# Kernel tuning notes

Measured on AMD Instinct MI355X. Metric: run time of the kernel, lower is better.

Reference implementation:

```python
import jax, jax.numpy as jnp
import numpy as np

B, N, F, C, E = 32768, 14, 128, 128, 64
NEG_SLOPE = 0.2

def setup_inputs() -> dict:
    key = jax.random.key(0)
    ks = jax.random.split(key, 14)
    feature = jax.random.normal(ks[0], (B, N, F), jnp.float32)
    src = jax.random.randint(ks[1], (B, E), 0, N)
    off = jax.random.randint(ks[2], (B, E), 1, N)
    dst = (src + off) % N  # guaranteed no self loops
    edge_list = jnp.stack([src, dst], axis=-1)  # [B,E,2] (src,dst) pairs
    s = 0.1
    return {
        'feature': feature,
        'edge_list': edge_list,
        'W1': jax.random.normal(ks[3], (F, C), jnp.float32) * s,
        'a_s1': jax.random.normal(ks[4], (C,), jnp.float32) * s,
        'a_d1': jax.random.normal(ks[5], (C,), jnp.float32) * s,
        'b1': jnp.zeros((C,), jnp.float32),
        'W2': jax.random.normal(ks[6], (C, C), jnp.float32) * s,
        'a_s2': jax.random.normal(ks[7], (C,), jnp.float32) * s,
        'a_d2': jax.random.normal(ks[8], (C,), jnp.float32) * s,
        'b2': jnp.zeros((C,), jnp.float32),
        'Wl': jax.random.normal(ks[9], (N * C, C // 2), jnp.float32) * 0.02,
        'bl': jnp.zeros((C // 2,), jnp.float32),
        'Wp': jax.random.normal(ks[10], (C // 2, 1), jnp.float32) * 0.02,
        'bp': jnp.zeros((1,), jnp.float32),
    }

def _gat_layer(x, W, a_s, a_d, b, src, dst):
    # x: [B,N,Fin]; src,dst: [B,Et] (self loops included). PyG GATConv, 1 head.
    Bn, Nn, _ = x.shape
    Et = src.shape[1]
    h = x @ W                                   # [B,N,C]
    as_n = jnp.einsum('bnc,c->bn', h, a_s)      # per-node src score
    ad_n = jnp.einsum('bnc,c->bn', h, a_d)      # per-node dst score
    logit = jax.nn.leaky_relu(
        jnp.take_along_axis(as_n, src, axis=1) + jnp.take_along_axis(ad_n, dst, axis=1),
        NEG_SLOPE)                               # [B,Et]
    # edge softmax grouped by (graph, dst) via flat segment ids
    seg = (jnp.arange(Bn)[:, None] * Nn + dst).reshape(-1)   # [B*Et]
    lf = logit.reshape(-1)
    m = jnp.full((Bn * Nn,), -jnp.inf, lf.dtype).at[seg].max(lf)
    e = jnp.exp(lf - m[seg])
    z = jnp.zeros((Bn * Nn,), lf.dtype).at[seg].add(e)
    alpha = e / z[seg]                           # [B*Et]
    Cc = h.shape[-1]
    msg = jnp.take_along_axis(h, src[..., None], axis=1).reshape(Bn * Et, Cc) * alpha[:, None]
    out = jnp.zeros((Bn * Nn, Cc), h.dtype).at[seg].add(msg).reshape(Bn, Nn, Cc) + b
    return out, alpha.reshape(Bn, Et)

def reference(feature, edge_list, W1, a_s1, a_d1, b1, W2, a_s2, a_d2, b2, Wl, bl, Wp, bp):
    Bn = feature.shape[0]
    sl = jnp.broadcast_to(jnp.arange(N)[None, :], (Bn, N))
    src = jnp.concatenate([edge_list[..., 0], sl], axis=1)   # [B,E+N]
    dst = jnp.concatenate([edge_list[..., 1], sl], axis=1)
    h1, _ = _gat_layer(feature, W1, a_s1, a_d1, b1, src, dst)
    h1 = jax.nn.relu(h1)                         # dropout p=0 (eval)
    h2, alpha = _gat_layer(h1, W2, a_s2, a_d2, b2, src, dst)
    attn = jnp.zeros((Bn, N, N), feature.dtype).at[jnp.arange(Bn)[:, None], src, dst].set(alpha)
    x = h2.reshape(Bn, N * C) @ Wl + bl
    pred = jax.nn.sigmoid(x @ Wp + bp)           # [B,1]
    return pred, attn
```

## Files before the change

### kernel.cpp

```cpp
#include <hip/hip_runtime.h>


#define NEG_SLOPE 0.2f

typedef __bf16 bf16x8 __attribute__((ext_vector_type(8)));
typedef float f32x4 __attribute__((ext_vector_type(4)));
typedef unsigned short us4v __attribute__((ext_vector_type(4)));
typedef unsigned short us8v __attribute__((ext_vector_type(8)));

static __device__ __forceinline__ unsigned short f2bf(float f) {
  unsigned u = __builtin_bit_cast(unsigned, f);
  return (unsigned short)((u + 0x7FFFu + ((u >> 16) & 1u)) >> 16);
}

__global__ void gat_setup_kernel(const float* __restrict__ W1, const float* __restrict__ W2,
                                 const float* __restrict__ Wl, const float* __restrict__ bl,
                                 const float* __restrict__ Wp, const float* __restrict__ bp,
                                 unsigned short* __restrict__ wfrag, float* __restrict__ weffc) {
  const int blk = blockIdx.x, tid = threadIdx.x;
  if (blk < 16) {
    int slot = blk * 256 + tid;
    int lane = slot & 63, t = (slot >> 6) & 7, ks = (slot >> 9) & 3, lr = slot >> 11;
    const float* W = lr ? W2 : W1;
    int q = lane >> 4, l = lane & 15;
    int n = t * 16 + l, k0 = ks * 32 + q * 8;
    us8v hv;
    #pragma unroll
    for (int j = 0; j < 8; ++j) hv[j] = f2bf(W[(k0 + j) * 128 + n]);
    *(us8v*)(wfrag + slot * 8) = hv;
  } else {
    for (int i = tid; i < 2048; i += 256) {
      int r = i & 3, lane = (i >> 2) & 63, t = i >> 8;
      int q = lane >> 4, l = lane & 15;
      int row = 4 * q + r, col = t * 16 + l;
      float s = 0.f;
      if (row < 14) {
        const float* wl = Wl + (size_t)(row * 128 + col) * 64;
        #pragma unroll 8
        for (int c = 0; c < 64; ++c) s += wl[c] * Wp[c];
      }
      weffc[i] = s;
    }
    if (tid == 0) {
      float s = 0.f;
      for (int c = 0; c < 64; ++c) s += bl[c] * Wp[c];
      weffc[2048] = s + bp[0];
    }
  }
}

struct __align__(16) WaveLds {
  unsigned short xh[3072];
  unsigned short Pb[384];
  float Pf[256];
  float asn[16], adn[16], mz[16];
  float attn[196];
};

__global__ __launch_bounds__(256, 4) void gat_kernel(
    const float* __restrict__ feat, const int* __restrict__ edges,
    const float* __restrict__ as1v, const float* __restrict__ ad1v,
    const float* __restrict__ b1v, const float* __restrict__ as2v,
    const float* __restrict__ ad2v, const float* __restrict__ b2v,
    const unsigned short* __restrict__ wfrag, const float* __restrict__ weffc,
    float* __restrict__ out) {
  __shared__ WaveLds wls[4];
  const int tid = threadIdx.x;
  const int wave = tid >> 6, lane = tid & 63;
  const int q = lane >> 4, l = lane & 15;
  const int g = blockIdx.x * 4 + wave;
  WaveLds& S = wls[wave];

  int esrc, edst;
  { const int2 e2 = *(const int2*)(edges + (size_t)g * 128 + lane * 2); esrc = e2.x; edst = e2.y; }

  us8v z8v = {0, 0, 0, 0, 0, 0, 0, 0};
  const bf16x8 zf = __builtin_bit_cast(bf16x8, z8v);

  bf16x8 af1[4];
  if (l < 14) {
    const float* fb = feat + (size_t)g * 1792 + l * 128 + q * 8;
    #pragma unroll
    for (int ks = 0; ks < 4; ++ks) {
      f32x4 v0 = *(const f32x4*)(fb + ks * 32);
      f32x4 v1 = *(const f32x4*)(fb + ks * 32 + 4);
      us8v hv;
      hv[0] = f2bf(v0[0]); hv[1] = f2bf(v0[1]); hv[2] = f2bf(v0[2]); hv[3] = f2bf(v0[3]);
      hv[4] = f2bf(v1[0]); hv[5] = f2bf(v1[1]); hv[6] = f2bf(v1[2]); hv[7] = f2bf(v1[3]);
      af1[ks] = __builtin_bit_cast(bf16x8, hv);
    }
  } else {
    #pragma unroll
    for (int ks = 0; ks < 4; ++ks) af1[ks] = zf;
  }

  f32x4 oacc[8];

  for (int lr = 0; lr < 2; ++lr) {
    const float* asv = lr ? as2v : as1v;
    const float* adv = lr ? ad2v : ad1v;
    const float* bsv = lr ? b2v : b1v;
    const unsigned short* wfl = wfrag + lr * 16384;

    f32x4 hacc[8];
    #pragma unroll
    for (int t = 0; t < 8; ++t) hacc[t] = (f32x4){0.f, 0.f, 0.f, 0.f};
    #pragma unroll
    for (int ks = 0; ks < 4; ++ks) {
      bf16x8 af = lr ? *(const bf16x8*)(&S.xh[l * 136 + ks * 32 + q * 8]) : af1[ks];
      const unsigned short* wk = wfl + ks * 4096 + lane * 8;
      #pragma unroll
      for (int t = 0; t < 8; ++t) {
        bf16x8 bfv = *(const bf16x8*)(wk + t * 512);
        hacc[t] = __builtin_amdgcn_mfma_f32_16x16x32_bf16(af, bfv, hacc[t], 0, 0, 0);
      }
    }

    f32x4 pas = {0.f, 0.f, 0.f, 0.f}, padv = {0.f, 0.f, 0.f, 0.f};
    #pragma unroll
    for (int t = 0; t < 8; ++t) {
      float ca = asv[t * 16 + l], cd = adv[t * 16 + l];
      pas += hacc[t] * ca;
      padv += hacc[t] * cd;
    }
    #pragma unroll
    for (int m = 1; m <= 8; m <<= 1) {
      #pragma unroll
      for (int r = 0; r < 4; ++r) {
        pas[r] += __shfl_xor(pas[r], m, 64);
        padv[r] += __shfl_xor(padv[r], m, 64);
      }
    }
    if (l == 0) {
      #pragma unroll
      for (int r = 0; r < 4; ++r) { S.asn[4 * q + r] = pas[r]; S.adn[4 * q + r] = padv[r]; }
    }

    #pragma unroll
    for (int t = 0; t < 8; ++t) {
      us4v hv;
      hv[0] = f2bf(hacc[t][0]); hv[1] = f2bf(hacc[t][1]);
      hv[2] = f2bf(hacc[t][2]); hv[3] = f2bf(hacc[t][3]);
      *(us4v*)(&S.xh[(t * 16 + l) * 24 + q * 4]) = hv;
    }
    *(f32x4*)(&S.Pf[lane * 4]) = (f32x4){0.f, 0.f, 0.f, 0.f};
    if (lr) { for (int i = lane; i < 196; i += 64) S.attn[i] = 0.f; }
    __threadfence_block();

    float ev, ev2 = 0.f;
    {
      float f = S.asn[esrc] + S.adn[edst];
      ev = __expf(f > 0.f ? f : NEG_SLOPE * f);
      atomicAdd(&S.Pf[edst * 16 + esrc], ev);
      if (lane < 14) {
        float f2 = S.asn[lane] + S.adn[lane];
        ev2 = __expf(f2 > 0.f ? f2 : NEG_SLOPE * f2);
        atomicAdd(&S.Pf[lane * 17], ev2);
      }
    }
    __threadfence_block();

    if (lane < 16) {
      f32x4 s0 = *(const f32x4*)(&S.Pf[lane * 16]) + *(const f32x4*)(&S.Pf[lane * 16 + 4]) +
                 *(const f32x4*)(&S.Pf[lane * 16 + 8]) + *(const f32x4*)(&S.Pf[lane * 16 + 12]);
      float z = s0[0] + s0[1] + s0[2] + s0[3];
      S.mz[lane] = (lane < 14) ? 1.f / z : 0.f;
    }
    __threadfence_block();

    #pragma unroll
    for (int i = lane; i < 256; i += 64) {
      int r = i >> 4, c = i & 15;
      float pv = S.Pf[i] * S.mz[r];
      S.Pb[r * 24 + c] = (r < 14 && c < 14) ? f2bf(pv) : (unsigned short)0;
    }
    if (lr) {
      S.attn[esrc * 14 + edst] = ev * S.mz[edst];
      if (lane < 14) S.attn[lane * 15] = ev2 * S.mz[lane];
    }
    __threadfence_block();

    #pragma unroll
    for (int t = 0; t < 8; ++t) {
      float bb = bsv[t * 16 + l];
      oacc[t] = (f32x4){bb, bb, bb, bb};
    }
    bf16x8 paf = (q < 2) ? *(const bf16x8*)(&S.Pb[l * 24 + q * 8]) : zf;
    #pragma unroll
    for (int t = 0; t < 8; ++t) {
      bf16x8 hbf = (q < 2) ? *(const bf16x8*)(&S.xh[(t * 16 + l) * 24 + q * 8]) : zf;
      oacc[t] = __builtin_amdgcn_mfma_f32_16x16x32_bf16(paf, hbf, oacc[t], 0, 0, 0);
    }

    if (lr == 0) {
      __threadfence_block();
      #pragma unroll
      for (int t = 0; t < 8; ++t) {
        #pragma unroll
        for (int r = 0; r < 4; ++r) {
          float v = fmaxf(oacc[t][r], 0.f);
          S.xh[(4 * q + r) * 136 + t * 16 + l] = f2bf(v);
        }
      }
      __threadfence_block();
    }
  }

  float part = 0.f;
  #pragma unroll
  for (int t = 0; t < 8; ++t) {
    f32x4 wv = *(const f32x4*)(weffc + t * 256 + lane * 4);
    part += oacc[t][0] * wv[0] + oacc[t][1] * wv[1] + oacc[t][2] * wv[2] + oacc[t][3] * wv[3];
  }
  #pragma unroll
  for (int m = 1; m < 64; m <<= 1) part += __shfl_xor(part, m, 64);
  if (lane == 0) {
    float p = 1.f / (1.f + __expf(-(part + weffc[2048])));
    out[g] = p;
  }

  {
    float* oa = out + 32768 + (size_t)g * 196;
    for (int i = lane; i < 196; i += 64) oa[i] = S.attn[i];
  }
}

extern "C" void kernel_launch(void* const* d_in, const int* in_sizes, int n_in,
                              void* d_out, int out_size, void* d_ws, size_t ws_size,
                              hipStream_t stream) {
  const float* feat = (const float*)d_in[0];
  const int* edges = (const int*)d_in[1];
  const float* W1 = (const float*)d_in[2];
  const float* as1 = (const float*)d_in[3];
  const float* ad1 = (const float*)d_in[4];
  const float* b1 = (const float*)d_in[5];
  const float* W2 = (const float*)d_in[6];
  const float* as2 = (const float*)d_in[7];
  const float* ad2 = (const float*)d_in[8];
  const float* b2 = (const float*)d_in[9];
  const float* Wl = (const float*)d_in[10];
  const float* bl = (const float*)d_in[11];
  const float* Wp = (const float*)d_in[12];
  const float* bp = (const float*)d_in[13];

  unsigned short* wfrag = (unsigned short*)d_ws;
  float* weffc = (float*)((char*)d_ws + 65536);

  gat_setup_kernel<<<17, 256, 0, stream>>>(W1, W2, Wl, bl, Wp, bp, wfrag, weffc);
  gat_kernel<<<8192, 256, 0, stream>>>(feat, edges, as1, ad1, b1, as2, ad2, b2,
                                       wfrag, weffc, (float*)d_out);
}
```

Baseline: 482.6 us.

## Stage bf16 weight fragments in LDS per 16-wave block, recompute attention from edge mask

Each block now runs 1024 threads (16 graphs) and first copies both layers' bf16 weight fragments (64 KB) into shared memory, so the MFMA B-operand loads come from LDS rather than global/L2. Feature loads are issued before the weight copy and barrier to overlap latency. The per-wave attention buffer is removed: an edge bitmask built with atomicOr lets the final attention matrix be recomputed from node scores and softmax normalisers at write-out. LDS strides are also shrunk. The cost is one block-wide barrier per block and larger LDS use, which may limit occupancy, plus some recomputation of exponentials.

Measured after the change: 490.7 us. Within noise of the previous version (+1.7%).

```diff
diff --git a/kernel.cpp b/kernel.cpp
--- a/kernel.cpp
+++ b/kernel.cpp
@@ -50,48 +50,67 @@
 }
 
 struct __align__(16) WaveLds {
-  unsigned short xh[3072];
-  unsigned short Pb[384];
-  float Pf[256];
+  unsigned short xh[2176];
+  unsigned short Pb[256];
+  float Pf[224];
   float asn[16], adn[16], mz[16];
-  float attn[196];
+  int emask[16];
 };
 
-__global__ __launch_bounds__(256, 4) void gat_kernel(
+__global__ __launch_bounds__(1024, 4) void gat_kernel(
     const float* __restrict__ feat, const int* __restrict__ edges,
     const float* __restrict__ as1v, const float* __restrict__ ad1v,
     const float* __restrict__ b1v, const float* __restrict__ as2v,
     const float* __restrict__ ad2v, const float* __restrict__ b2v,
     const unsigned short* __restrict__ wfrag, const float* __restrict__ weffc,
     float* __restrict__ out) {
-  __shared__ WaveLds wls[4];
+  __shared__ unsigned short sW[32768];
+  __shared__ WaveLds wls[16];
+
   const int tid = threadIdx.x;
   const int wave = tid >> 6, lane = tid & 63;
   const int q = lane >> 4, l = lane & 15;
-  const int g = blockIdx.x * 4 + wave;
+  const int g = blockIdx.x * 16 + wave;
   WaveLds& S = wls[wave];
 
+  f32x4 fv[8];
+  if (l < 14) {
+    const float* fb = feat + (size_t)g * 1792 + l * 128 + q * 8;
+    #pragma unroll
+    for (int ks = 0; ks < 4; ++ks) {
+      fv[2 * ks] = *(const f32x4*)(fb + ks * 32);
+      fv[2 * ks + 1] = *(const f32x4*)(fb + ks * 32 + 4);
+    }
+  } else {
+    #pragma unroll
+    for (int c = 0; c < 8; ++c) fv[c] = (f32x4){0.f, 0.f, 0.f, 0.f};
+  }
   int esrc, edst;
   { const int2 e2 = *(const int2*)(edges + (size_t)g * 128 + lane * 2); esrc = e2.x; edst = e2.y; }
+  if (lane < 16) S.emask[lane] = 0;
+
+  #pragma unroll
+  for (int it = 0; it < 4; ++it) {
+    int off = it * 1024 + tid;
+    *(us8v*)(&sW[off * 8]) = *(const us8v*)(wfrag + off * 8);
+  }
+  __syncthreads();
+
+  atomicOr(&S.emask[esrc], 1 << edst);
+  if (lane < 14) atomicOr(&S.emask[lane], 1 << lane);
 
   us8v z8v = {0, 0, 0, 0, 0, 0, 0, 0};
   const bf16x8 zf = __builtin_bit_cast(bf16x8, z8v);
 
   bf16x8 af1[4];
-  if (l < 14) {
-    const float* fb = feat + (size_t)g * 1792 + l * 128 + q * 8;
-    #pragma unroll
-    for (int ks = 0; ks < 4; ++ks) {
-      f32x4 v0 = *(const f32x4*)(fb + ks * 32);
-      f32x4 v1 = *(const f32x4*)(fb + ks * 32 + 4);
-      us8v hv;
-      hv[0] = f2bf(v0[0]); hv[1] = f2bf(v0[1]); hv[2] = f2bf(v0[2]); hv[3] = f2bf(v0[3]);
-      hv[4] = f2bf(v1[0]); hv[5] = f2bf(v1[1]); hv[6] = f2bf(v1[2]); hv[7] = f2bf(v1[3]);
-      af1[ks] = __builtin_bit_cast(bf16x8, hv);
-    }
-  } else {
-    #pragma unroll
-    for (int ks = 0; ks < 4; ++ks) af1[ks] = zf;
+  #pragma unroll
+  for (int ks = 0; ks < 4; ++ks) {
+    us8v hv;
+    hv[0] = f2bf(fv[2 * ks][0]); hv[1] = f2bf(fv[2 * ks][1]);
+    hv[2] = f2bf(fv[2 * ks][2]); hv[3] = f2bf(fv[2 * ks][3]);
+    hv[4] = f2bf(fv[2 * ks + 1][0]); hv[5] = f2bf(fv[2 * ks + 1][1]);
+    hv[6] = f2bf(fv[2 * ks + 1][2]); hv[7] = f2bf(fv[2 * ks + 1][3]);
+    af1[ks] = __builtin_bit_cast(bf16x8, hv);
   }
 
   f32x4 oacc[8];
@@ -100,7 +119,6 @@
     const float* asv = lr ? as2v : as1v;
     const float* adv = lr ? ad2v : ad1v;
     const float* bsv = lr ? b2v : b1v;
-    const unsigned short* wfl = wfrag + lr * 16384;
 
     f32x4 hacc[8];
     #pragma unroll
@@ -108,7 +126,7 @@
     #pragma unroll
     for (int ks = 0; ks < 4; ++ks) {
       bf16x8 af = lr ? *(const bf16x8*)(&S.xh[l * 136 + ks * 32 + q * 8]) : af1[ks];
-      const unsigned short* wk = wfl + ks * 4096 + lane * 8;
+      const unsigned short* wk = sW + (lr * 4 + ks) * 4096 + lane * 8;
       #pragma unroll
       for (int t = 0; t < 8; ++t) {
         bf16x8 bfv = *(const bf16x8*)(wk + t * 512);
@@ -141,42 +159,31 @@
       us4v hv;
       hv[0] = f2bf(hacc[t][0]); hv[1] = f2bf(hacc[t][1]);
       hv[2] = f2bf(hacc[t][2]); hv[3] = f2bf(hacc[t][3]);
-      *(us4v*)(&S.xh[(t * 16 + l) * 24 + q * 4]) = hv;
-    }
-    *(f32x4*)(&S.Pf[lane * 4]) = (f32x4){0.f, 0.f, 0.f, 0.f};
-    if (lr) { for (int i = lane; i < 196; i += 64) S.attn[i] = 0.f; }
-    __threadfence_block();
-
-    float ev, ev2 = 0.f;
-    {
-      float f = S.asn[esrc] + S.adn[edst];
-      ev = __expf(f > 0.f ? f : NEG_SLOPE * f);
-      atomicAdd(&S.Pf[edst * 16 + esrc], ev);
-      if (lane < 14) {
-        float f2 = S.asn[lane] + S.adn[lane];
-        ev2 = __expf(f2 > 0.f ? f2 : NEG_SLOPE * f2);
-        atomicAdd(&S.Pf[lane * 17], ev2);
-      }
-    }
-    __threadfence_block();
-
-    if (lane < 16) {
+      *(us4v*)(&S.xh[(t * 16 + l) * 16 + q * 4]) = hv;
+    }
+    if (lane < 56) *(f32x4*)(&S.Pf[lane * 4]) = (f32x4){0.f, 0.f, 0.f, 0.f};
+    __threadfence_block();
+
+    float f0 = S.asn[esrc] + S.adn[edst];
+    float ev = __expf(f0 > 0.f ? f0 : NEG_SLOPE * f0);
+    atomicAdd(&S.Pf[edst * 16 + esrc], ev);
+    if (lane < 14) {
+      float f2 = S.asn[lane] + S.adn[lane];
+      atomicAdd(&S.Pf[lane * 17], __expf(f2 > 0.f ? f2 : NEG_SLOPE * f2));
+    }
+    __threadfence_block();
+
+    if (lane < 14) {
       f32x4 s0 = *(const f32x4*)(&S.Pf[lane * 16]) + *(const f32x4*)(&S.Pf[lane * 16 + 4]) +
                  *(const f32x4*)(&S.Pf[lane * 16 + 8]) + *(const f32x4*)(&S.Pf[lane * 16 + 12]);
-      float z = s0[0] + s0[1] + s0[2] + s0[3];
-      S.mz[lane] = (lane < 14) ? 1.f / z : 0.f;
+      S.mz[lane] = 1.f / (s0[0] + s0[1] + s0[2] + s0[3]);
     }
     __threadfence_block();
 
     #pragma unroll
     for (int i = lane; i < 256; i += 64) {
       int r = i >> 4, c = i & 15;
-      float pv = S.Pf[i] * S.mz[r];
-      S.Pb[r * 24 + c] = (r < 14 && c < 14) ? f2bf(pv) : (unsigned short)0;
-    }
-    if (lr) {
-      S.attn[esrc * 14 + edst] = ev * S.mz[edst];
-      if (lane < 14) S.attn[lane * 15] = ev2 * S.mz[lane];
+      S.Pb[i] = (r < 14 && c < 14) ? f2bf(S.Pf[i] * S.mz[r]) : (unsigned short)0;
     }
     __threadfence_block();
 
@@ -185,10 +192,10 @@
       float bb = bsv[t * 16 + l];
       oacc[t] = (f32x4){bb, bb, bb, bb};
     }
-    bf16x8 paf = (q < 2) ? *(const bf16x8*)(&S.Pb[l * 24 + q * 8]) : zf;
-    #pragma unroll
-    for (int t = 0; t < 8; ++t) {
-      bf16x8 hbf = (q < 2) ? *(const bf16x8*)(&S.xh[(t * 16 + l) * 24 + q * 8]) : zf;
+    bf16x8 paf = (q < 2) ? *(const bf16x8*)(&S.Pb[l * 16 + q * 8]) : zf;
+    #pragma unroll
+    for (int t = 0; t < 8; ++t) {
+      bf16x8 hbf = (q < 2) ? *(const bf16x8*)(&S.xh[(t * 16 + l) * 16 + q * 8]) : zf;
       oacc[t] = __builtin_amdgcn_mfma_f32_16x16x32_bf16(paf, hbf, oacc[t], 0, 0, 0);
     }
 
@@ -214,14 +221,24 @@
   }
   #pragma unroll
   for (int m = 1; m < 64; m <<= 1) part += __shfl_xor(part, m, 64);
-  if (lane == 0) {
-    float p = 1.f / (1.f + __expf(-(part + weffc[2048])));
-    out[g] = p;
-  }
+  if (lane == 0) out[g] = 1.f / (1.f + __expf(-(part + weffc[2048])));
 
   {
     float* oa = out + 32768 + (size_t)g * 196;
-    for (int i = lane; i < 196; i += 64) oa[i] = S.attn[i];
+    #pragma unroll
+    for (int k = 0; k < 4; ++k) {
+      int i = lane + k * 64;
+      if (i < 196) {
+        int s = (i * 4682) >> 16;
+        int d = i - s * 14;
+        float a = 0.f;
+        if ((S.emask[s] >> d) & 1) {
+          float f = S.asn[s] + S.adn[d];
+          a = __expf(f > 0.f ? f : NEG_SLOPE * f) * S.mz[d];
+        }
+        oa[i] = a;
+      }
+    }
   }
 }
 
@@ -247,6 +264,6 @@
   float* weffc = (float*)((char*)d_ws + 65536);
 
   gat_setup_kernel<<<17, 256, 0, stream>>>(W1, W2, Wl, bl, Wp, bp, wfrag, weffc);
-  gat_kernel<<<8192, 256, 0, stream>>>(feat, edges, as1, ad1, b1, as2, ad2, b2,
-                                       wfrag, weffc, (float*)d_out);
-}
+  gat_kernel<<<2048, 1024, 0, stream>>>(feat, edges, as1, ad1, b1, as2, ad2, b2,
+                                        wfrag, weffc, (float*)d_out);
+}
```
